# Performance work log

Measured on AMD Instinct MI355X. Metric: run time of the kernel, lower is better.

Reference implementation:

```python
import jax, jax.numpy as jnp
import numpy as np

IGNORE_INDEX = -100


def setup_inputs() -> dict:
    key = jax.random.key(0)
    k_e, k_c, k_t = jax.random.split(key, 3)
    B, T, D, V = 1, 8192, 1024, 50257
    e = jax.random.normal(k_e, (B, T, D), dtype=jnp.float32)
    c = jax.random.normal(k_c, (V, D), dtype=jnp.float32) * (D ** -0.5)
    targets = jax.random.randint(k_t, (B, T), 0, V, dtype=jnp.int64)
    bias = jnp.zeros((V,), dtype=jnp.float32)
    return {"e": e, "c": c, "targets": targets, "bias": bias}


def _linear_cross_entropy(e, c, bias, targets, ignore_index=IGNORE_INDEX,
                          softcap=None, reduction="mean"):
    B, T, D = e.shape
    V = c.shape[0]
    ef = e.reshape(B * T, D)
    tf = targets.reshape(B * T)
    # logits: [N, V] = e @ c^T + bias
    logits = jnp.einsum("nd,vd->nv", ef, c) + bias
    if softcap is not None:
        logits = softcap * jnp.tanh(logits / softcap)
    # stable cross entropy: lse - logit[target]
    lse = jax.nn.logsumexp(logits, axis=-1)  # [N]
    safe_t = jnp.where(tf == ignore_index, 0, tf)
    tgt_logit = jnp.take_along_axis(logits, safe_t[:, None], axis=-1)[:, 0]
    nll = lse - tgt_logit  # [N]
    valid = (tf != ignore_index)
    nll = jnp.where(valid, nll, 0.0)
    if reduction == "mean":
        denom = jnp.maximum(valid.sum().astype(nll.dtype), 1.0)
        return nll.sum() / denom
    elif reduction == "sum":
        return nll.sum()
    else:  # 'none'
        return nll.reshape(B, T)


def reference(e, c, targets, bias):
    return _linear_cross_entropy(e, c, bias, targets)
```

## Files before the change

### kernel.cpp

```cpp
#include <hip/hip_runtime.h>
#include <hip/hip_bf16.h>
#include <math.h>


#define BM 128
#define BN 128
#define BKB 128

typedef int   i32x8 __attribute__((ext_vector_type(8)));
typedef float f32x4 __attribute__((ext_vector_type(4)));

__device__ __forceinline__ void load_lds16(const void* g, void* l) {
    __builtin_amdgcn_global_load_lds(
        (const __attribute__((address_space(1))) void*)g,
        (__attribute__((address_space(3))) void*)l, 16, 0, 0);
}

__device__ __forceinline__ unsigned char f2e4m3_sw(float x) {
    unsigned u = __float_as_uint(x);
    unsigned s = (u >> 24) & 0x80;
    float ax = __uint_as_float(u & 0x7fffffff);
    if (ax != ax) return (unsigned char)(s | 0x7f);
    if (ax >= 448.f) return (unsigned char)(s | 0x7e);
    if (ax < 0.0009765625f) return (unsigned char)s;
    if (ax < 0.015625f) {
        int n = (int)rintf(ax * 512.f);
        return (unsigned char)(s | n);
    }
    int e = (int)((u >> 23) & 0xff) - 127;
    unsigned m = u & 0x7fffff;
    unsigned keep = m >> 20, rest = m & 0xfffff;
    if (rest > 0x80000u || (rest == 0x80000u && (keep & 1))) keep++;
    if (keep == 8) { keep = 0; e++; if (e > 8) return (unsigned char)(s | 0x7e); }
    return (unsigned char)(s | ((e + 7) << 3) | keep);
}

__device__ __forceinline__ unsigned int pk4_fp8(float a, float b, float c, float d) {
#if __has_builtin(__builtin_amdgcn_cvt_pk_fp8_f32)
    int v = __builtin_amdgcn_cvt_pk_fp8_f32(a, b, 0, false);
    v = __builtin_amdgcn_cvt_pk_fp8_f32(c, d, v, true);
    return (unsigned int)v;
#else
    return (unsigned int)f2e4m3_sw(a) | ((unsigned int)f2e4m3_sw(b) << 8) |
           ((unsigned int)f2e4m3_sw(c) << 16) | ((unsigned int)f2e4m3_sw(d) << 24);
#endif
}

__global__ void cast_all_fp8(const float* __restrict__ e,
                             const float* __restrict__ c,
                             unsigned char* __restrict__ e_f8,
                             unsigned char* __restrict__ c_f8,
                             long ne, long ncs, long ncd) {
    long i8 = ((long)blockIdx.x * blockDim.x + threadIdx.x) * 8;
    if (i8 >= ne + ncd) return;
    const float* src;
    unsigned char* dst;
    float scale;
    bool zero = false;
    if (i8 < ne) {
        src = e + i8; dst = e_f8 + i8; scale = 1.0f;
    } else {
        long j8 = i8 - ne;
        dst = c_f8 + j8; scale = 16.0f;
        src = c + j8;
        zero = (j8 + 7 >= ncs);
    }
    uint2 o;
    if (!zero) {
        float4 v0 = *(const float4*)(src);
        float4 v1 = *(const float4*)(src + 4);
        o.x = pk4_fp8(v0.x * scale, v0.y * scale, v0.z * scale, v0.w * scale);
        o.y = pk4_fp8(v1.x * scale, v1.y * scale, v1.z * scale, v1.w * scale);
    } else {
        o.x = o.y = 0u;
    }
    *(uint2*)dst = o;
}

__global__ __launch_bounds__(256)
void gemm_lse_partial(const unsigned char* __restrict__ E,
                      const unsigned char* __restrict__ C,
                      const float* __restrict__ bias,
                      const int* __restrict__ targets,
                      float* __restrict__ row_sum,
                      float* __restrict__ tgt,
                      int N, int D, int V) {
    __shared__ unsigned char As[BM * BKB];
    __shared__ unsigned char Bs[BN * BKB];
    __shared__ float bias_s[BN];
    __shared__ int tgt_s[BM];
    __shared__ float red_s[2][BM];

    const int t = threadIdx.x;
    const int w = t >> 6;
    const int l = t & 63;
    const int quad = l >> 4;
    const int lm = l & 15;
    const int wr0 = (w >> 1) * 64;
    const int wc0 = (w & 1) * 64;

    const int mt = blockIdx.x;
    const int vt = blockIdx.y;

    if (t < BN) {
        int col = vt * BN + t;
        bias_s[t] = (col < V) ? bias[col] : -INFINITY;
    }
    if (t >= BN && t < BN + BM)
        tgt_s[t - BN] = targets[mt * BM + (t - BN)];

    const int srow = t >> 3;
    const int schunk = (t & 7) ^ (srow & 7);
    const unsigned char* ga = E + (long)(mt * BM + srow) * D + schunk * 16;
    const unsigned char* gb = C + (long)(vt * BN + srow) * D + schunk * 16;
    char* lA = (char*)As + w * 1024;
    char* lB = (char*)Bs + w * 1024;
    const long rnd = 32L * D;

    f32x4 acc[4][4] = {};
    const int sA = 127;
    const int sB = 123;

    for (int k0 = 0; k0 < D; k0 += BKB) {
#pragma unroll
        for (int ro = 0; ro < 4; ro++) {
            load_lds16(ga + k0 + ro * rnd, lA + ro * 4096);
            load_lds16(gb + k0 + ro * rnd, lB + ro * 4096);
        }
        __syncthreads();

        const int c0 = ((quad << 1) ^ (lm & 7)) << 4;
        const int c1 = c0 ^ 16;
        i32x8 a_frag[4], b_frag[4];
#pragma unroll
        for (int ti = 0; ti < 4; ti++) {
            const unsigned char* pr = As + (wr0 + ti * 16 + lm) * 128;
            int4 lo = *(const int4*)(pr + c0);
            int4 hi = *(const int4*)(pr + c1);
            a_frag[ti] = (i32x8){lo.x, lo.y, lo.z, lo.w, hi.x, hi.y, hi.z, hi.w};
        }
#pragma unroll
        for (int tj = 0; tj < 4; tj++) {
            const unsigned char* pr = Bs + (wc0 + tj * 16 + lm) * 128;
            int4 lo = *(const int4*)(pr + c0);
            int4 hi = *(const int4*)(pr + c1);
            b_frag[tj] = (i32x8){lo.x, lo.y, lo.z, lo.w, hi.x, hi.y, hi.z, hi.w};
        }
#pragma unroll
        for (int ti = 0; ti < 4; ti++)
#pragma unroll
            for (int tj = 0; tj < 4; tj++)
                acc[ti][tj] = __builtin_amdgcn_mfma_scale_f32_16x16x128_f8f6f4(
                    a_frag[ti], b_frag[tj], acc[ti][tj], 0, 0, 0, sA, 0, sB);
        __syncthreads();
    }

    float bvals[4];
#pragma unroll
    for (int tj = 0; tj < 4; tj++) bvals[tj] = bias_s[wc0 + tj * 16 + lm];

#pragma unroll
    for (int ti = 0; ti < 4; ti++) {
#pragma unroll
        for (int r = 0; r < 4; r++) {
            const int row_local = wr0 + ti * 16 + quad * 4 + r;
            const int tl = tgt_s[row_local] - vt * BN;
            float srow_ = 0.f;
#pragma unroll
            for (int tj = 0; tj < 4; tj++) {
                float v = acc[ti][tj][r] + bvals[tj];
                srow_ += __expf(v);
                if (wc0 + tj * 16 + lm == tl)
                    tgt[mt * BM + row_local] = v;
            }
#pragma unroll
            for (int off = 1; off < 16; off <<= 1)
                srow_ += __shfl_xor(srow_, off, 64);
            if (lm == 0)
                red_s[w & 1][row_local] = srow_;
        }
    }
    __syncthreads();
    if (t < BM)
        atomicAdd(&row_sum[(long)mt * BM + t], red_s[0][t] + red_s[1][t]);
}

__global__ void lse_finish(const float* __restrict__ row_sum,
                           const float* __restrict__ tgt,
                           const int* __restrict__ targets,
                           float* __restrict__ gacc, int N) {
    __shared__ float sred[8];
    int r = blockIdx.x * 256 + threadIdx.x;
    float nll = 0.f, cnt = 0.f;
    if (r < N) {
        int tg = targets[r];
        if (tg != -100) { nll = logf(row_sum[r]) - tgt[r]; cnt = 1.f; }
    }
#pragma unroll
    for (int off = 32; off; off >>= 1) {
        nll += __shfl_xor(nll, off, 64);
        cnt += __shfl_xor(cnt, off, 64);
    }
    int w = threadIdx.x >> 6, l = threadIdx.x & 63;
    if (l == 0) { sred[w] = nll; sred[4 + w] = cnt; }
    __syncthreads();
    if (threadIdx.x == 0) {
        atomicAdd(gacc, sred[0] + sred[1] + sred[2] + sred[3]);
        atomicAdd(gacc + 1, sred[4] + sred[5] + sred[6] + sred[7]);
    }
}

__global__ void final_scalar(const float* __restrict__ gacc, float* __restrict__ out) {
    out[0] = gacc[0] / fmaxf(gacc[1], 1.f);
}

extern "C" void kernel_launch(void* const* d_in, const int* in_sizes, int n_in,
                              void* d_out, int out_size, void* d_ws, size_t ws_size,
                              hipStream_t stream) {
    const float* e       = (const float*)d_in[0];
    const float* c       = (const float*)d_in[1];
    const int*   targets = (const int*)d_in[2];
    const float* bias    = (const float*)d_in[3];
    float* out = (float*)d_out;

    const int N = in_sizes[2];
    const int V = in_sizes[3];
    const int D = in_sizes[0] / N;
    const int mtiles = N / BM;
    const int vtiles = (V + BN - 1) / BN;
    const long Vpad = (long)vtiles * BN;

    char* ws = (char*)d_ws;
    size_t off = 0;
    auto alloc = [&](size_t bytes) {
        void* p = ws + off;
        off += (bytes + 255) & ~(size_t)255;
        return p;
    };
    unsigned char* e_f8 = (unsigned char*)alloc((size_t)N * D);
    unsigned char* c_f8 = (unsigned char*)alloc((size_t)Vpad * D);
    float* row_sum = (float*)alloc((size_t)N * 4);
    float* gacc    = (float*)alloc(8);
    float* tgt     = (float*)alloc((size_t)N * 4);

    hipMemsetAsync(row_sum, 0, (size_t)N * 4 + 256 + 8, stream);

    const long ne  = (long)N * D;
    const long ncs = (long)V * D;
    const long ncd = Vpad * D;
    const long tot8 = (ne + ncd) / 8;
    cast_all_fp8<<<(int)((tot8 + 255) / 256), 256, 0, stream>>>(
        e, c, e_f8, c_f8, ne, ncs, ncd);

    dim3 grid(mtiles, vtiles);
    gemm_lse_partial<<<grid, 256, 0, stream>>>(e_f8, c_f8, bias, targets,
                                               row_sum, tgt, N, D, V);

    lse_finish<<<(N + 255) / 256, 256, 0, stream>>>(row_sum, tgt, targets, gacc, N);
    final_scalar<<<1, 1, 0, stream>>>(gacc, out);
}
```

Baseline: 821.7 us.

## Fuse LSE finish and final reduction into GEMM via last-block counters; drop memset

The final LSE/NLL reduction and the scalar mean are folded into the GEMM kernel. Per-m-tile atomic counters pick the last v-tile block, which finishes its rows, and a global counter lets the last m-tile write the output. Zeroing of the accumulators moves into the cast kernel, so the memset and two launches go away. The LDS tile layout is also changed to two 64-byte K halves with a new swizzle to alter bank access. This adds atomic counter traffic and more complex memory-ordering logic.

```diff
diff --git a/kernel.cpp b/kernel.cpp
--- a/kernel.cpp
+++ b/kernel.cpp
@@ -50,8 +50,11 @@
                              const float* __restrict__ c,
                              unsigned char* __restrict__ e_f8,
                              unsigned char* __restrict__ c_f8,
+                             unsigned int* __restrict__ zbase, int zwords,
                              long ne, long ncs, long ncd) {
-    long i8 = ((long)blockIdx.x * blockDim.x + threadIdx.x) * 8;
+    long tid = (long)blockIdx.x * blockDim.x + threadIdx.x;
+    if (tid < zwords) zbase[tid] = 0u;
+    long i8 = tid * 8;
     if (i8 >= ne + ncd) return;
     const float* src;
     unsigned char* dst;
@@ -78,18 +81,24 @@
 }
 
 __global__ __launch_bounds__(256)
-void gemm_lse_partial(const unsigned char* __restrict__ E,
-                      const unsigned char* __restrict__ C,
-                      const float* __restrict__ bias,
-                      const int* __restrict__ targets,
-                      float* __restrict__ row_sum,
-                      float* __restrict__ tgt,
-                      int N, int D, int V) {
-    __shared__ unsigned char As[BM * BKB];
-    __shared__ unsigned char Bs[BN * BKB];
+void gemm_lse_fused(const unsigned char* __restrict__ E,
+                    const unsigned char* __restrict__ C,
+                    const float* __restrict__ bias,
+                    const int* __restrict__ targets,
+                    float* __restrict__ row_sum,
+                    float* __restrict__ tgt,
+                    float* __restrict__ gacc,
+                    int* __restrict__ done,
+                    int* __restrict__ mt_cnt,
+                    float* __restrict__ out,
+                    int N, int D, int V, int vtiles, int mtiles) {
+    __shared__ unsigned char As[2 * BM * 64];
+    __shared__ unsigned char Bs[2 * BN * 64];
     __shared__ float bias_s[BN];
     __shared__ int tgt_s[BM];
     __shared__ float red_s[2][BM];
+    __shared__ float fin[8];
+    __shared__ int is_last;
 
     const int t = threadIdx.x;
     const int w = t >> 6;
@@ -109,41 +118,44 @@
     if (t >= BN && t < BN + BM)
         tgt_s[t - BN] = targets[mt * BM + (t - BN)];
 
-    const int srow = t >> 3;
-    const int schunk = (t & 7) ^ (srow & 7);
-    const unsigned char* ga = E + (long)(mt * BM + srow) * D + schunk * 16;
-    const unsigned char* gb = C + (long)(vt * BN + srow) * D + schunk * 16;
+    const int schunk = (t & 3) ^ ((t >> 3) & 3);
+    const unsigned char* ga = E + (long)(mt * BM + (t >> 2)) * D + schunk * 16;
+    const unsigned char* gb = C + (long)(vt * BN + (t >> 2)) * D + schunk * 16;
     char* lA = (char*)As + w * 1024;
     char* lB = (char*)Bs + w * 1024;
-    const long rnd = 32L * D;
+    const long roff0 = 0, roff1 = 64L * D, roff2 = 64, roff3 = 64L * D + 64;
 
     f32x4 acc[4][4] = {};
     const int sA = 127;
     const int sB = 123;
 
     for (int k0 = 0; k0 < D; k0 += BKB) {
-#pragma unroll
-        for (int ro = 0; ro < 4; ro++) {
-            load_lds16(ga + k0 + ro * rnd, lA + ro * 4096);
-            load_lds16(gb + k0 + ro * rnd, lB + ro * 4096);
-        }
+        load_lds16(ga + k0 + roff0, lA);
+        load_lds16(ga + k0 + roff1, lA + 4096);
+        load_lds16(ga + k0 + roff2, lA + 8192);
+        load_lds16(ga + k0 + roff3, lA + 12288);
+        load_lds16(gb + k0 + roff0, lB);
+        load_lds16(gb + k0 + roff1, lB + 4096);
+        load_lds16(gb + k0 + roff2, lB + 8192);
+        load_lds16(gb + k0 + roff3, lB + 12288);
         __syncthreads();
 
-        const int c0 = ((quad << 1) ^ (lm & 7)) << 4;
-        const int c1 = c0 ^ 16;
+        const int h_off = (quad >> 1) * 8192;
+        const int s0 = (((quad & 1) << 1) ^ ((lm >> 1) & 3)) << 4;
+        const int s1 = s0 ^ 16;
         i32x8 a_frag[4], b_frag[4];
 #pragma unroll
         for (int ti = 0; ti < 4; ti++) {
-            const unsigned char* pr = As + (wr0 + ti * 16 + lm) * 128;
-            int4 lo = *(const int4*)(pr + c0);
-            int4 hi = *(const int4*)(pr + c1);
+            const unsigned char* pr = As + h_off + (wr0 + ti * 16 + lm) * 64;
+            int4 lo = *(const int4*)(pr + s0);
+            int4 hi = *(const int4*)(pr + s1);
             a_frag[ti] = (i32x8){lo.x, lo.y, lo.z, lo.w, hi.x, hi.y, hi.z, hi.w};
         }
 #pragma unroll
         for (int tj = 0; tj < 4; tj++) {
-            const unsigned char* pr = Bs + (wc0 + tj * 16 + lm) * 128;
-            int4 lo = *(const int4*)(pr + c0);
-            int4 hi = *(const int4*)(pr + c1);
+            const unsigned char* pr = Bs + h_off + (wc0 + tj * 16 + lm) * 64;
+            int4 lo = *(const int4*)(pr + s0);
+            int4 hi = *(const int4*)(pr + s1);
             b_frag[tj] = (i32x8){lo.x, lo.y, lo.z, lo.w, hi.x, hi.y, hi.z, hi.w};
         }
 #pragma unroll
@@ -164,14 +176,15 @@
 #pragma unroll
         for (int r = 0; r < 4; r++) {
             const int row_local = wr0 + ti * 16 + quad * 4 + r;
-            const int tl = tgt_s[row_local] - vt * BN;
+            const int tl = tgt_s[row_local] - vt * BN - wc0;
             float srow_ = 0.f;
 #pragma unroll
             for (int tj = 0; tj < 4; tj++) {
                 float v = acc[ti][tj][r] + bvals[tj];
                 srow_ += __expf(v);
-                if (wc0 + tj * 16 + lm == tl)
-                    tgt[mt * BM + row_local] = v;
+                if (tj * 16 + lm == tl)
+                    __hip_atomic_store(&tgt[mt * BM + row_local], v,
+                                       __ATOMIC_RELAXED, __HIP_MEMORY_SCOPE_AGENT);
             }
 #pragma unroll
             for (int off = 1; off < 16; off <<= 1)
@@ -182,36 +195,50 @@
     }
     __syncthreads();
     if (t < BM)
-        atomicAdd(&row_sum[(long)mt * BM + t], red_s[0][t] + red_s[1][t]);
-}
-
-__global__ void lse_finish(const float* __restrict__ row_sum,
-                           const float* __restrict__ tgt,
-                           const int* __restrict__ targets,
-                           float* __restrict__ gacc, int N) {
-    __shared__ float sred[8];
-    int r = blockIdx.x * 256 + threadIdx.x;
-    float nll = 0.f, cnt = 0.f;
-    if (r < N) {
+        atomicAdd(&row_sum[mt * BM + t], red_s[0][t] + red_s[1][t]);
+    __syncthreads();
+
+    if (t == 0) {
+        int d = __hip_atomic_fetch_add(&mt_cnt[mt], 1,
+                                       __ATOMIC_ACQ_REL, __HIP_MEMORY_SCOPE_AGENT);
+        is_last = (d == vtiles - 1);
+    }
+    __syncthreads();
+    if (!is_last) return;
+
+    float nllv = 0.f, cntv = 0.f;
+    if (t < BM) {
+        int r = mt * BM + t;
         int tg = targets[r];
-        if (tg != -100) { nll = logf(row_sum[r]) - tgt[r]; cnt = 1.f; }
+        if (tg != -100) {
+            float s = __hip_atomic_load(&row_sum[r], __ATOMIC_RELAXED,
+                                        __HIP_MEMORY_SCOPE_AGENT);
+            float tv = __hip_atomic_load(&tgt[r], __ATOMIC_RELAXED,
+                                         __HIP_MEMORY_SCOPE_AGENT);
+            nllv = logf(s) - tv;
+            cntv = 1.f;
+        }
     }
 #pragma unroll
     for (int off = 32; off; off >>= 1) {
-        nll += __shfl_xor(nll, off, 64);
-        cnt += __shfl_xor(cnt, off, 64);
-    }
-    int w = threadIdx.x >> 6, l = threadIdx.x & 63;
-    if (l == 0) { sred[w] = nll; sred[4 + w] = cnt; }
-    __syncthreads();
-    if (threadIdx.x == 0) {
-        atomicAdd(gacc, sred[0] + sred[1] + sred[2] + sred[3]);
-        atomicAdd(gacc + 1, sred[4] + sred[5] + sred[6] + sred[7]);
-    }
-}
-
-__global__ void final_scalar(const float* __restrict__ gacc, float* __restrict__ out) {
-    out[0] = gacc[0] / fmaxf(gacc[1], 1.f);
+        nllv += __shfl_xor(nllv, off, 64);
+        cntv += __shfl_xor(cntv, off, 64);
+    }
+    if (l == 0) { fin[w] = nllv; fin[4 + w] = cntv; }
+    __syncthreads();
+    if (t == 0) {
+        atomicAdd(gacc,     fin[0] + fin[1] + fin[2] + fin[3]);
+        atomicAdd(gacc + 1, fin[4] + fin[5] + fin[6] + fin[7]);
+        int d = __hip_atomic_fetch_add(done, 1,
+                                       __ATOMIC_ACQ_REL, __HIP_MEMORY_SCOPE_AGENT);
+        if (d == mtiles - 1) {
+            float S = __hip_atomic_load(gacc, __ATOMIC_RELAXED,
+                                        __HIP_MEMORY_SCOPE_AGENT);
+            float Cn = __hip_atomic_load(gacc + 1, __ATOMIC_RELAXED,
+                                         __HIP_MEMORY_SCOPE_AGENT);
+            out[0] = S / fmaxf(Cn, 1.f);
+        }
+    }
 }
 
 extern "C" void kernel_launch(void* const* d_in, const int* in_sizes, int n_in,
@@ -239,23 +266,22 @@
     };
     unsigned char* e_f8 = (unsigned char*)alloc((size_t)N * D);
     unsigned char* c_f8 = (unsigned char*)alloc((size_t)Vpad * D);
-    float* row_sum = (float*)alloc((size_t)N * 4);
-    float* gacc    = (float*)alloc(8);
+    const int zwords = N + 2 + 1 + mtiles;
+    float* row_sum = (float*)alloc((size_t)zwords * 4);
+    float* gacc    = row_sum + N;
+    int*   done    = (int*)(row_sum + N + 2);
+    int*   mt_cnt  = (int*)(row_sum + N + 3);
     float* tgt     = (float*)alloc((size_t)N * 4);
-
-    hipMemsetAsync(row_sum, 0, (size_t)N * 4 + 256 + 8, stream);
 
     const long ne  = (long)N * D;
     const long ncs = (long)V * D;
     const long ncd = Vpad * D;
     const long tot8 = (ne + ncd) / 8;
     cast_all_fp8<<<(int)((tot8 + 255) / 256), 256, 0, stream>>>(
-        e, c, e_f8, c_f8, ne, ncs, ncd);
+        e, c, e_f8, c_f8, (unsigned int*)row_sum, zwords, ne, ncs, ncd);
 
     dim3 grid(mtiles, vtiles);
-    gemm_lse_partial<<<grid, 256, 0, stream>>>(e_f8, c_f8, bias, targets,
-                                               row_sum, tgt, N, D, V);
-
-    lse_finish<<<(N + 255) / 256, 256, 0, stream>>>(row_sum, tgt, targets, gacc, N);
-    final_scalar<<<1, 1, 0, stream>>>(gacc, out);
-}
+    gemm_lse_fused<<<grid, 256, 0, stream>>>(
+        e_f8, c_f8, bias, targets, row_sum, tgt, gacc, done, mt_cnt, out,
+        N, D, V, vtiles, mtiles);
+}
```

Measured after the change: 1.113 ms. +35.4%, slower.
